# Kernel optimization log

Hardware: AMD Instinct MI355X
Metric: run time of the kernel (lower is better)

Reference implementation:

```python
import jax, jax.numpy as jnp
import numpy as np

BATCH = 32768


def _unpack(packed, n):
    # packed: [rows, ceil(n/8)] ints in [0,256). Extract bits MSB-first per byte.
    bits = (packed[:, :, None] >> jnp.arange(7, -1, -1, dtype=packed.dtype)) & 1
    return bits.reshape(packed.shape[0], -1)[:, :n]  # [rows, n] of {0,1}


def setup_inputs() -> dict:
    key = jax.random.key(0)
    k0, k1, k2, k3, k4 = jax.random.split(key, 5)
    return {
        "x": jax.random.normal(k0, (BATCH, 784), dtype=jnp.float32),
        "w1_packed": jax.random.randint(k1, (256, 98), 0, 256, dtype=jnp.int32),
        "m1_packed": jax.random.randint(k2, (256, 98), 0, 256, dtype=jnp.int32),
        "alpha1": jnp.float32(1.0),
        "w2_packed": jax.random.randint(k3, (10, 32), 0, 256, dtype=jnp.int32),
        "m2_packed": jax.random.randint(k4, (10, 32), 0, 256, dtype=jnp.int32),
        "alpha2": jnp.float32(1.0),
    }


def reference(x, w1_packed, m1_packed, alpha1, w2_packed, m2_packed, alpha2):
    # Layer 1: binary {-1,+1} weights * {0,1} mask * alpha
    w1 = (2 * _unpack(w1_packed, 784) - 1).astype(jnp.float32)
    w1 = w1 * _unpack(m1_packed, 784).astype(jnp.float32) * alpha1  # [256, 784]
    h = jax.nn.relu(jnp.einsum('bi,oi->bo', x, w1))  # [B, 256]
    # Layer 2
    w2 = (2 * _unpack(w2_packed, 256) - 1).astype(jnp.float32)
    w2 = w2 * _unpack(m2_packed, 256).astype(jnp.float32) * alpha2  # [10, 256]
    return jnp.einsum('bh,oh->bo', h, w2)  # [B, 10]
```

## Files before the change

### kernel.cpp

```cpp
#include <hip/hip_runtime.h>
#include <hip/hip_bf16.h>

typedef __bf16 bf16x8 __attribute__((ext_vector_type(8)));
typedef float floatx4 __attribute__((ext_vector_type(4)));

__device__ __forceinline__ unsigned short f2bf(float f) {
  __bf16 b = (__bf16)f;
  return __builtin_bit_cast(unsigned short, b);
}

__global__ void decode_w1_kernel(const int* __restrict__ w1p,
                                 const int* __restrict__ m1p,
                                 unsigned short* __restrict__ w1t) {
  int t = blockIdx.x * 256 + threadIdx.x;
  int r = t & 255;
  int j = t >> 8;
  unsigned short vals[8];
#pragma unroll
  for (int k = 0; k < 8; ++k) vals[k] = 0;
  if (j < 98) {
    unsigned int v = (unsigned int)w1p[r * 98 + j];
    unsigned int m = (unsigned int)m1p[r * 98 + j];
#pragma unroll
    for (int k = 0; k < 8; ++k) {
      unsigned int bit = (v >> (7 - k)) & 1u;
      unsigned int mk  = (m >> (7 - k)) & 1u;
      vals[k] = (unsigned short)(mk ? (bit ? 0x3F80u : 0xBF80u) : 0u);
    }
  }
  uint4 pack;
  pack.x = (unsigned)vals[0] | ((unsigned)vals[1] << 16);
  pack.y = (unsigned)vals[2] | ((unsigned)vals[3] << 16);
  pack.z = (unsigned)vals[4] | ((unsigned)vals[5] << 16);
  pack.w = (unsigned)vals[6] | ((unsigned)vals[7] << 16);
  *reinterpret_cast<uint4*>(w1t + t * 8) = pack;
}

#define BM 32
#define HS_LD 264
#define W2_LD 264

#define OFF_W2 8448

__global__ __launch_bounds__(512, 8) void fused_kernel(
    const float* __restrict__ x,
    const unsigned short* __restrict__ w1t,
    const int* __restrict__ w2p,
    const int* __restrict__ m2p,
    const float* __restrict__ a1p,
    const float* __restrict__ a2p,
    float* __restrict__ out) {
  __shared__ unsigned short smem[13312];

  const int tid  = threadIdx.x;
  const int wave = tid >> 6;
  const int lane = tid & 63;
  const int l15  = lane & 15;
  const int quad = lane >> 4;
  const int row0 = blockIdx.x * BM;

  floatx4 acc[2][2];
#pragma unroll
  for (int i = 0; i < 2; ++i)
#pragma unroll
    for (int j = 0; j < 2; ++j) acc[i][j] = (floatx4){0.f, 0.f, 0.f, 0.f};

  const int sr = tid >> 4;
  const int g0 = tid & 15;
  const float* xrow = x + (size_t)(row0 + sr) * 784;

  auto stage_half = [&](int sp) {
    float4 xv[7];
#pragma unroll
    for (int it = 0; it < 7; ++it) {
      int g = g0 + it * 16;
      int col = sp * 416 + g * 4;
      if (g < 104 && col < 784)
        xv[it] = *reinterpret_cast<const float4*>(xrow + col);
      else
        xv[it] = (float4){0.f, 0.f, 0.f, 0.f};
    }
#pragma unroll
    for (int it = 0; it < 7; ++it) {
      int g = g0 + it * 16;
      if (g < 104) {
        ushort4 b;
        b.x = f2bf(xv[it].x); b.y = f2bf(xv[it].y);
        b.z = f2bf(xv[it].z); b.w = f2bf(xv[it].w);
        *reinterpret_cast<ushort4*>(&smem[(g >> 1) * 256 + sr * 8 + (g & 1) * 4]) = b;
      }
    }
  };

  const unsigned short* wl = w1t + ((size_t)wave * 32 + l15) * 8;

  auto compute_half = [&](int hb) {
#pragma unroll
    for (int cl = 0; cl < 13; ++cl) {
      const int cg = hb * 13 + cl;
      bf16x8 af[2], bfv[2];
#pragma unroll
      for (int nj = 0; nj < 2; ++nj)
        bfv[nj] = *reinterpret_cast<const bf16x8*>(
            wl + (size_t)(cg * 4 + quad) * 2048 + nj * 128);
#pragma unroll
      for (int mi = 0; mi < 2; ++mi)
        af[mi] = *reinterpret_cast<const bf16x8*>(
            &smem[(cl * 4 + quad) * 256 + (mi * 16 + l15) * 8]);
#pragma unroll
      for (int mi = 0; mi < 2; ++mi)
#pragma unroll
        for (int nj = 0; nj < 2; ++nj)
          acc[mi][nj] = __builtin_amdgcn_mfma_f32_16x16x32_bf16(
              af[mi], bfv[nj], acc[mi][nj], 0, 0, 0);
    }
  };

  stage_half(0);
  __syncthreads();
  compute_half(0);
  __syncthreads();
  stage_half(1);
  __syncthreads();
  compute_half(1);
  __syncthreads();

  const float a1 = a1p[0];
  const float a2 = a2p[0];
#pragma unroll
  for (int mi = 0; mi < 2; ++mi) {
#pragma unroll
    for (int nj = 0; nj < 2; ++nj) {
      int col   = wave * 32 + nj * 16 + l15;
      int rbase = mi * 16 + quad * 4;
#pragma unroll
      for (int rr = 0; rr < 4; ++rr) {
        float h = fmaxf(a1 * acc[mi][nj][rr], 0.f);
        smem[(rbase + rr) * HS_LD + col] = f2bf(h);
      }
    }
  }
  if (tid < 320) {
    int rr = tid >> 5, j = tid & 31;
    unsigned int v = (unsigned int)w2p[rr * 32 + j];
    unsigned int m = (unsigned int)m2p[rr * 32 + j];
#pragma unroll
    for (int k = 0; k < 8; ++k) {
      unsigned int bit = (v >> (7 - k)) & 1u;
      unsigned int mk  = (m >> (7 - k)) & 1u;
      smem[OFF_W2 + rr * W2_LD + j * 8 + k] =
          (unsigned short)(mk ? (bit ? 0x3F80u : 0xBF80u) : 0u);
    }
  }
  for (int idx = tid; idx < 6 * 256; idx += 512) {
    int rr = 10 + (idx >> 8), c = idx & 255;
    smem[OFF_W2 + rr * W2_LD + c] = 0;
  }
  __syncthreads();

  if (wave < 2) {
    floatx4 o2 = (floatx4){0.f, 0.f, 0.f, 0.f};
#pragma unroll
    for (int ks = 0; ks < 8; ++ks) {
      bf16x8 ha = *reinterpret_cast<const bf16x8*>(
          &smem[(wave * 16 + l15) * HS_LD + ks * 32 + quad * 8]);
      bf16x8 wb = *reinterpret_cast<const bf16x8*>(
          &smem[OFF_W2 + l15 * W2_LD + ks * 32 + quad * 8]);
      o2 = __builtin_amdgcn_mfma_f32_16x16x32_bf16(ha, wb, o2, 0, 0, 0);
    }
    if (l15 < 10) {
#pragma unroll
      for (int rr = 0; rr < 4; ++rr) {
        int gr = row0 + wave * 16 + quad * 4 + rr;
        out[(size_t)gr * 10 + l15] = a2 * o2[rr];
      }
    }
  }
}

extern "C" void kernel_launch(void* const* d_in, const int* in_sizes, int n_in,
                              void* d_out, int out_size, void* d_ws, size_t ws_size,
                              hipStream_t stream) {
  const float* x   = (const float*)d_in[0];
  const int*   w1p = (const int*)d_in[1];
  const int*   m1p = (const int*)d_in[2];
  const float* a1  = (const float*)d_in[3];
  const int*   w2p = (const int*)d_in[4];
  const int*   m2p = (const int*)d_in[5];
  const float* a2  = (const float*)d_in[6];
  unsigned short* w1t = (unsigned short*)d_ws;
  float* out = (float*)d_out;

  decode_w1_kernel<<<104, 256, 0, stream>>>(w1p, m1p, w1t);
  fused_kernel<<<1024, 512, 0, stream>>>(x, w1t, w2p, m2p, a1, a2, out);
}
```

Before: 176.3 us.

## Pre-convert x to bf16 MFMA-friendly layout and stream fragments from global memory

Adds a separate kernel that converts x to bf16 in a k-chunk-major layout matching the MFMA fragment order. The fused kernel then loads A and B fragments directly from global memory with register double-buffered prefetch instead of staging through LDS, and the row tile grows from 32 to 64 rows. This removes the LDS staging and barriers in the main loop. In exchange it adds a full extra write and read of a bf16 copy of x through HBM, which for a memory-bound kernel may cost more than it saves.

```diff
diff --git a/kernel.cpp b/kernel.cpp
--- a/kernel.cpp
+++ b/kernel.cpp
@@ -36,21 +36,41 @@
   *reinterpret_cast<uint4*>(w1t + t * 8) = pack;
 }
 
-#define BM 32
+__global__ __launch_bounds__(256, 4) void xform_x_kernel(
+    const float* __restrict__ x,
+    unsigned short* __restrict__ xt) {
+  const int kq = blockIdx.x >> 7;
+  const int r  = ((blockIdx.x & 127) << 8) + threadIdx.x;
+  uint4 pack;
+  if (kq < 98) {
+    const float* p = x + (size_t)r * 784 + kq * 8;
+    float4 a = *reinterpret_cast<const float4*>(p);
+    float4 b = *reinterpret_cast<const float4*>(p + 4);
+    pack.x = (unsigned)f2bf(a.x) | ((unsigned)f2bf(a.y) << 16);
+    pack.y = (unsigned)f2bf(a.z) | ((unsigned)f2bf(a.w) << 16);
+    pack.z = (unsigned)f2bf(b.x) | ((unsigned)f2bf(b.y) << 16);
+    pack.w = (unsigned)f2bf(b.z) | ((unsigned)f2bf(b.w) << 16);
+  } else {
+    pack = (uint4){0u, 0u, 0u, 0u};
+  }
+  *reinterpret_cast<uint4*>(xt + ((size_t)kq * 32768 + r) * 8) = pack;
+}
+
+#define BM 64
+#define NCH 25
 #define HS_LD 264
 #define W2_LD 264
+#define OFF_W2 16896
 
-#define OFF_W2 8448
-
-__global__ __launch_bounds__(512, 8) void fused_kernel(
-    const float* __restrict__ x,
+__global__ __launch_bounds__(512, 4) void fused_kernel(
+    const unsigned short* __restrict__ xt,
     const unsigned short* __restrict__ w1t,
     const int* __restrict__ w2p,
     const int* __restrict__ m2p,
     const float* __restrict__ a1p,
     const float* __restrict__ a2p,
     float* __restrict__ out) {
-  __shared__ unsigned short smem[13312];
+  __shared__ unsigned short smem[64 * HS_LD + 16 * W2_LD];
 
   const int tid  = threadIdx.x;
   const int wave = tid >> 6;
@@ -59,76 +79,46 @@
   const int quad = lane >> 4;
   const int row0 = blockIdx.x * BM;
 
-  floatx4 acc[2][2];
+  floatx4 acc[4][2];
 #pragma unroll
-  for (int i = 0; i < 2; ++i)
+  for (int i = 0; i < 4; ++i)
 #pragma unroll
     for (int j = 0; j < 2; ++j) acc[i][j] = (floatx4){0.f, 0.f, 0.f, 0.f};
 
-  const int sr = tid >> 4;
-  const int g0 = tid & 15;
-  const float* xrow = x + (size_t)(row0 + sr) * 784;
+  const unsigned short* xl = xt + ((size_t)quad * 32768 + row0 + l15) * 8;
+  const unsigned short* wl = w1t + ((size_t)quad * 256 + wave * 32 + l15) * 8;
 
-  auto stage_half = [&](int sp) {
-    float4 xv[7];
+  bf16x8 afb[2][4], bfb[2][2];
+  auto pref = [&](int kc, int b) {
 #pragma unroll
-    for (int it = 0; it < 7; ++it) {
-      int g = g0 + it * 16;
-      int col = sp * 416 + g * 4;
-      if (g < 104 && col < 784)
-        xv[it] = *reinterpret_cast<const float4*>(xrow + col);
-      else
-        xv[it] = (float4){0.f, 0.f, 0.f, 0.f};
-    }
+    for (int mi = 0; mi < 4; ++mi)
+      afb[b][mi] = *reinterpret_cast<const bf16x8*>(
+          xl + (size_t)kc * 1048576 + mi * 128);
 #pragma unroll
-    for (int it = 0; it < 7; ++it) {
-      int g = g0 + it * 16;
-      if (g < 104) {
-        ushort4 b;
-        b.x = f2bf(xv[it].x); b.y = f2bf(xv[it].y);
-        b.z = f2bf(xv[it].z); b.w = f2bf(xv[it].w);
-        *reinterpret_cast<ushort4*>(&smem[(g >> 1) * 256 + sr * 8 + (g & 1) * 4]) = b;
-      }
-    }
+    for (int nj = 0; nj < 2; ++nj)
+      bfb[b][nj] = *reinterpret_cast<const bf16x8*>(
+          wl + (size_t)kc * 8192 + nj * 128);
+  };
+  auto mm = [&](int b) {
+#pragma unroll
+    for (int mi = 0; mi < 4; ++mi)
+#pragma unroll
+      for (int nj = 0; nj < 2; ++nj)
+        acc[mi][nj] = __builtin_amdgcn_mfma_f32_16x16x32_bf16(
+            afb[b][mi], bfb[b][nj], acc[mi][nj], 0, 0, 0);
   };
 
-  const unsigned short* wl = w1t + ((size_t)wave * 32 + l15) * 8;
-
-  auto compute_half = [&](int hb) {
+  pref(0, 0);
 #pragma unroll
-    for (int cl = 0; cl < 13; ++cl) {
-      const int cg = hb * 13 + cl;
-      bf16x8 af[2], bfv[2];
-#pragma unroll
-      for (int nj = 0; nj < 2; ++nj)
-        bfv[nj] = *reinterpret_cast<const bf16x8*>(
-            wl + (size_t)(cg * 4 + quad) * 2048 + nj * 128);
-#pragma unroll
-      for (int mi = 0; mi < 2; ++mi)
-        af[mi] = *reinterpret_cast<const bf16x8*>(
-            &smem[(cl * 4 + quad) * 256 + (mi * 16 + l15) * 8]);
-#pragma unroll
-      for (int mi = 0; mi < 2; ++mi)
-#pragma unroll
-        for (int nj = 0; nj < 2; ++nj)
-          acc[mi][nj] = __builtin_amdgcn_mfma_f32_16x16x32_bf16(
-              af[mi], bfv[nj], acc[mi][nj], 0, 0, 0);
-    }
-  };
-
-  stage_half(0);
-  __syncthreads();
-  compute_half(0);
-  __syncthreads();
-  stage_half(1);
-  __syncthreads();
-  compute_half(1);
-  __syncthreads();
+  for (int kc = 0; kc < NCH; ++kc) {
+    if (kc + 1 < NCH) pref(kc + 1, (kc + 1) & 1);
+    mm(kc & 1);
+  }
 
   const float a1 = a1p[0];
   const float a2 = a2p[0];
 #pragma unroll
-  for (int mi = 0; mi < 2; ++mi) {
+  for (int mi = 0; mi < 4; ++mi) {
 #pragma unroll
     for (int nj = 0; nj < 2; ++nj) {
       int col   = wave * 32 + nj * 16 + l15;
@@ -158,7 +148,7 @@
   }
   __syncthreads();
 
-  if (wave < 2) {
+  if (wave < 4) {
     floatx4 o2 = (floatx4){0.f, 0.f, 0.f, 0.f};
 #pragma unroll
     for (int ks = 0; ks < 8; ++ks) {
@@ -189,8 +179,10 @@
   const int*   m2p = (const int*)d_in[5];
   const float* a2  = (const float*)d_in[6];
   unsigned short* w1t = (unsigned short*)d_ws;
+  unsigned short* xt  = (unsigned short*)((char*)d_ws + 425984);
   float* out = (float*)d_out;
 
   decode_w1_kernel<<<104, 256, 0, stream>>>(w1p, m1p, w1t);
-  fused_kernel<<<1024, 512, 0, stream>>>(x, w1t, w2p, m2p, a1, a2, out);
+  xform_x_kernel<<<100 * 128, 256, 0, stream>>>(x, xt);
+  fused_kernel<<<512, 512, 0, stream>>>(xt, w1t, w2p, m2p, a1, a2, out);
 }
```

Measured after the change: 202.9 us. 1.15x slower.
